# Kernel tuning notes

Hardware: AMD Instinct MI355X
Metric: run time of the kernel (lower is better)

## Reference

```python
import jax, jax.numpy as jnp
import numpy as np
import math

EMBED = 1024
HEADS = 16
HEAD_DIM = 64
HIDDEN = 4 * EMBED
EPS = 1e-5


def setup_inputs() -> dict:
    key = jax.random.key(0)
    ks = jax.random.split(key, 12)
    B, T, C = 2, 2048, EMBED
    s = 0.02
    return {
        "x": jax.random.normal(ks[0], (B, T, C), jnp.float32),
        "ln1_g": jnp.ones((C,), jnp.float32),
        "ln1_b": jnp.zeros((C,), jnp.float32),
        "qkv_w": jax.random.normal(ks[1], (C, 3 * C), jnp.float32) * s,
        "qkv_b": jnp.zeros((3 * C,), jnp.float32),
        "out_w": jax.random.normal(ks[2], (C, C), jnp.float32) * s,
        "out_b": jnp.zeros((C,), jnp.float32),
        "ln2_g": jnp.ones((C,), jnp.float32),
        "ln2_b": jnp.zeros((C,), jnp.float32),
        "fc1_w": jax.random.normal(ks[3], (C, HIDDEN), jnp.float32) * s,
        "fc1_b": jnp.zeros((HIDDEN,), jnp.float32),
        "fc2_w": jax.random.normal(ks[4], (HIDDEN, C), jnp.float32) * s,
        "fc2_b": jnp.zeros((C,), jnp.float32),
    }


def _layernorm(x, g, b):
    mu = jnp.mean(x, axis=-1, keepdims=True)
    var = jnp.var(x, axis=-1, keepdims=True)
    return (x - mu) * jax.lax.rsqrt(var + EPS) * g + b


def _attention(x, qkv_w, qkv_b, out_w, out_b):
    B, T, C = x.shape
    qkv = x @ qkv_w + qkv_b  # [B,T,3C]
    q, k, v = jnp.split(qkv, 3, axis=-1)
    # [B,H,T,hd]
    def heads(t):
        return t.reshape(B, T, HEADS, HEAD_DIM).transpose(0, 2, 1, 3)
    q, k, v = heads(q), heads(k), heads(v)
    scale = 1.0 / math.sqrt(HEAD_DIM)
    attn = jnp.einsum('bhqd,bhkd->bhqk', q, k) * scale
    causal = jnp.triu(jnp.ones((T, T), bool), k=1)
    attn = jnp.where(causal, -jnp.inf, attn)
    attn = jax.nn.softmax(attn, axis=-1)
    out = jnp.einsum('bhqk,bhkd->bhqd', attn, v)
    out = out.transpose(0, 2, 1, 3).reshape(B, T, C)
    return out @ out_w + out_b


def reference(x, ln1_g, ln1_b, qkv_w, qkv_b, out_w, out_b, ln2_g, ln2_b, fc1_w, fc1_b, fc2_w, fc2_b):
    x = x + _attention(_layernorm(x, ln1_g, ln1_b), qkv_w, qkv_b, out_w, out_b)
    h = _layernorm(x, ln2_g, ln2_b)
    h = jax.nn.gelu(h @ fc1_w + fc1_b, approximate=False) @ fc2_w + fc2_b
    return x + h
```

## Files before the change

kernel.cpp:

```cpp
#include <hip/hip_runtime.h>
#include <hip/hip_bf16.h>
#include <math.h>

typedef float f32x4 __attribute__((ext_vector_type(4)));
typedef __bf16 bf16x8 __attribute__((ext_vector_type(8)));
typedef __hip_bfloat16 bf16;

constexpr int T_SEQ = 2048;
constexpr int C_EMB = 1024;
constexpr int N_HEAD = 16;
constexpr int D_HEAD = 64;
constexpr int BATCH = 2;
constexpr int M_ROWS = BATCH * T_SEQ;
constexpr int HIDDEN_DIM = 4096;

static __device__ __forceinline__ f32x4 zero4() {
  f32x4 z; z[0] = 0.f; z[1] = 0.f; z[2] = 0.f; z[3] = 0.f; return z;
}

static __device__ __forceinline__ void gl_lds16(const bf16* g, bf16* l) {
  __builtin_amdgcn_global_load_lds(
      (const __attribute__((address_space(1))) unsigned int*)g,
      (__attribute__((address_space(3))) unsigned int*)l, 16, 0, 0);
}

#define BAR() asm volatile("s_barrier" ::: "memory")

__global__ __launch_bounds__(256) void ln_kernel(const float* __restrict__ x,
                                                 const float* __restrict__ gamma,
                                                 const float* __restrict__ beta,
                                                 bf16* __restrict__ out) {
  int row = blockIdx.x;
  const float* xr = x + (size_t)row * C_EMB;
  int t = threadIdx.x;
  float4 v = *(const float4*)&xr[t * 4];
  float s = v.x + v.y + v.z + v.w;
  float ss = v.x * v.x + v.y * v.y + v.z * v.z + v.w * v.w;
#pragma unroll
  for (int off = 32; off > 0; off >>= 1) {
    s += __shfl_down(s, off, 64);
    ss += __shfl_down(ss, off, 64);
  }
  __shared__ float sbuf[8];
  int w = t >> 6;
  if ((t & 63) == 0) { sbuf[w] = s; sbuf[4 + w] = ss; }
  __syncthreads();
  s = sbuf[0] + sbuf[1] + sbuf[2] + sbuf[3];
  ss = sbuf[4] + sbuf[5] + sbuf[6] + sbuf[7];
  float mu = s * (1.0f / C_EMB);
  float var = ss * (1.0f / C_EMB) - mu * mu;
  float rstd = rsqrtf(var + 1e-5f);
  float4 g4 = *(const float4*)&gamma[t * 4];
  float4 b4 = *(const float4*)&beta[t * 4];
  bf16* orow = out + (size_t)row * C_EMB + t * 4;
  orow[0] = __float2bfloat16((v.x - mu) * rstd * g4.x + b4.x);
  orow[1] = __float2bfloat16((v.y - mu) * rstd * g4.y + b4.y);
  orow[2] = __float2bfloat16((v.z - mu) * rstd * g4.z + b4.z);
  orow[3] = __float2bfloat16((v.w - mu) * rstd * g4.w + b4.w);
}

__global__ __launch_bounds__(256) void cast_transpose_all(
    const float* __restrict__ qkv_w, bf16* __restrict__ Wqkv,
    const float* __restrict__ out_w, bf16* __restrict__ Wout,
    const float* __restrict__ fc1_w, bf16* __restrict__ W1,
    const float* __restrict__ fc2_w, bf16* __restrict__ W2) {
  int id = blockIdx.x;
  const float* src; bf16* dst; int K, N, tt;
  if (id < 3072)      { src = qkv_w; dst = Wqkv; K = 1024; N = 3072; tt = id; }
  else if (id < 4096) { src = out_w; dst = Wout; K = 1024; N = 1024; tt = id - 3072; }
  else if (id < 8192) { src = fc1_w; dst = W1;   K = 1024; N = 4096; tt = id - 4096; }
  else                { src = fc2_w; dst = W2;   K = 4096; N = 1024; tt = id - 8192; }
  int ntx = N >> 5;
  int n0 = (tt % ntx) * 32, k0 = (tt / ntx) * 32;
  __shared__ float tile[32][33];
  int tx = threadIdx.x & 31, ty = threadIdx.x >> 5;
#pragma unroll
  for (int i = 0; i < 4; ++i)
    tile[ty + 8 * i][tx] = src[(size_t)(k0 + ty + 8 * i) * N + n0 + tx];
  __syncthreads();
#pragma unroll
  for (int i = 0; i < 4; ++i)
    dst[(size_t)(n0 + ty + 8 * i) * K + k0 + tx] = __float2bfloat16(tile[tx][ty + 8 * i]);
}

__global__ __launch_bounds__(256) void transpose_v(const bf16* __restrict__ V,
                                                   bf16* __restrict__ Vt) {
  int tt = blockIdx.x, bh = blockIdx.y;
  __shared__ bf16 tile[64][72];
  const bf16* src = V + ((size_t)bh * T_SEQ + tt * 64) * 64;
  int t = threadIdx.x;
  for (int idx = t; idx < 512; idx += 256) {
    int r = idx >> 3, c = (idx & 7) * 8;
    *(int4*)&tile[r][c] = *(const int4*)&src[r * 64 + c];
  }
  __syncthreads();
  bf16* dst = Vt + ((size_t)bh * 64) * T_SEQ + tt * 64;
  for (int idx = t; idx < 512; idx += 256) {
    int d = idx >> 3, c = (idx & 7) * 8;
    union { bf16 h[8]; int4 v; } u;
#pragma unroll
    for (int j = 0; j < 8; ++j) u.h[j] = tile[c + j][d];
    *(int4*)&dst[(size_t)d * T_SEQ + c] = u.v;
  }
}

template <int EPI>
__global__ __launch_bounds__(512) void gemm8p(
    const bf16* __restrict__ A, const bf16* __restrict__ Bt,
    const float* __restrict__ bias, int M, int N, int K,
    bf16* __restrict__ out_b16,
    bf16* __restrict__ q_out, bf16* __restrict__ k_out, bf16* __restrict__ v_out) {
  constexpr int NFR = 4;
  __shared__ bf16 Asl[2][2][128 * 64];
  __shared__ bf16 Bsl[2][2][128 * 64];

  int gx = gridDim.x, nwg = gx * gridDim.y;
  int flat = blockIdx.y * gx + blockIdx.x;
  int swz = (flat & 7) * (nwg >> 3) + (flat >> 3);
  int bx = swz % gx, by = swz / gx;

  int m0 = by * 256, n0 = bx * 256;
  int t = threadIdx.x;
  int wv = t >> 6, lane = t & 63, g = lane >> 4, r16 = lane & 15;
  int wm = wv >> 2, wn = wv & 3;

  f32x4 acc[8][NFR];
#pragma unroll
  for (int i = 0; i < 8; ++i)
#pragma unroll
    for (int j = 0; j < NFR; ++j) acc[i][j] = zero4();

  int lrow8 = lane >> 3;
  int srcg = (lane & 7) ^ lrow8;
  int NT = K / 64;

  auto stageA = [&](int tile, int h) {
    int par = tile & 1;
    const bf16* base = A + (size_t)(m0 + h * 128) * K + tile * 64;
#pragma unroll
    for (int j = 0; j < 2; ++j) {
      const bf16* src = base + (size_t)((wv * 2 + j) * 8 + lrow8) * K + srcg * 8;
      gl_lds16(src, &Asl[par][h][((wv * 2 + j) * 8) * 64]);
    }
  };
  auto stageB = [&](int tile, int h) {
    int par = tile & 1;
    const bf16* base = Bt + (size_t)(n0 + h * 128) * K + tile * 64;
#pragma unroll
    for (int j = 0; j < 2; ++j) {
      const bf16* src = base + (size_t)((wv * 2 + j) * 8 + lrow8) * K + srcg * 8;
      gl_lds16(src, &Bsl[par][h][((wv * 2 + j) * 8) * 64]);
    }
  };

  int xk[2];
#pragma unroll
  for (int kk = 0; kk < 2; ++kk) xk[kk] = (((kk * 4 + g) ^ (r16 & 7)) << 3);
  int bhalf = wn >> 1;
  int blrow0 = (wn & 1) * 64;

  stageA(0, 0); stageA(0, 1); stageB(0, 0); stageB(0, 1);
  if (NT > 1) {
    stageB(1, 0); stageB(1, 1);
    asm volatile("s_waitcnt vmcnt(4)" ::: "memory");
  } else {
    asm volatile("s_waitcnt vmcnt(0)" ::: "memory");
  }
  BAR();

  bf16x8 bfr[NFR][2];

  for (int u = 0; u < NT; ++u) {
    int par = u & 1;
    const bf16* Ab = &Asl[par][wm][0];
    const bf16* Bb = &Bsl[par][bhalf][0];
#pragma unroll
    for (int q = 0; q < 4; ++q) {
      if (q == 0) {
#pragma unroll
        for (int ni = 0; ni < NFR; ++ni)
#pragma unroll
          for (int kk = 0; kk < 2; ++kk)
            bfr[ni][kk] = *(const bf16x8*)&Bb[(blrow0 + ni * 16 + r16) * 64 + xk[kk]];
      }
      bf16x8 af[2][2];
#pragma unroll
      for (int d = 0; d < 2; ++d)
#pragma unroll
        for (int kk = 0; kk < 2; ++kk)
          af[d][kk] = *(const bf16x8*)&Ab[((2 * q + d) * 16 + r16) * 64 + xk[kk]];
      if (q == 0) { if (u + 1 < NT) stageA(u + 1, 0); }
      else if (q == 1) { if (u + 1 < NT) stageA(u + 1, 1); }
      else if (q == 2) { if (u + 2 < NT) stageB(u + 2, 0); }
      else { if (u + 2 < NT) stageB(u + 2, 1); }
      BAR();
      asm volatile("s_waitcnt lgkmcnt(0)" ::: "memory");
      __builtin_amdgcn_sched_barrier(0);
      __builtin_amdgcn_s_setprio(1);
#pragma unroll
      for (int d = 0; d < 2; ++d)
#pragma unroll
        for (int ni = 0; ni < NFR; ++ni) {
          acc[2 * q + d][ni] = __builtin_amdgcn_mfma_f32_16x16x32_bf16(af[d][0], bfr[ni][0], acc[2 * q + d][ni], 0, 0, 0);
          acc[2 * q + d][ni] = __builtin_amdgcn_mfma_f32_16x16x32_bf16(af[d][1], bfr[ni][1], acc[2 * q + d][ni], 0, 0, 0);
        }
      __builtin_amdgcn_s_setprio(0);
      if (q == 3) {
        if (u + 2 < NT)
          asm volatile("s_waitcnt vmcnt(4)" ::: "memory");
        else
          asm volatile("s_waitcnt vmcnt(0)" ::: "memory");
      }
      BAR();
    }
  }

#pragma unroll
  for (int mi = 0; mi < 8; ++mi) {
#pragma unroll
    for (int ni = 0; ni < NFR; ++ni) {
      int col = n0 + wn * 64 + ni * 16 + r16;
      float bv = bias[col];
#pragma unroll
      for (int reg = 0; reg < 4; ++reg) {
        int row = m0 + wm * 128 + mi * 16 + g * 4 + reg;
        float v = acc[mi][ni][reg] + bv;
        if constexpr (EPI == 0) {
          int part = col >> 10, cc = col & 1023;
          int hh = cc >> 6, dd = cc & 63;
          int bb = row >> 11, tt2 = row & 2047;
          size_t idx = (((size_t)bb * N_HEAD + hh) * T_SEQ + tt2) * D_HEAD + dd;
          if (part == 0) q_out[idx] = __float2bfloat16(v * 0.125f);
          else if (part == 1) k_out[idx] = __float2bfloat16(v);
          else v_out[idx] = __float2bfloat16(v);
        } else {
          float ge = 0.5f * v * (1.0f + erff(v * 0.70710678118f));
          out_b16[(size_t)row * N + col] = __float2bfloat16(ge);
        }
      }
    }
  }
}

__global__ __launch_bounds__(256) void gemmW(
    const bf16* __restrict__ A, const bf16* __restrict__ Bt,
    const float* __restrict__ bias, int M, int N, int K,
    const float* __restrict__ res, float* __restrict__ out_f32) {
  __shared__ bf16 Abuf[2][128 * 64];
  __shared__ bf16 Bbuf[2][64 * 64];

  int gx = gridDim.x, nwg = gx * gridDim.y;
  int flat = blockIdx.y * gx + blockIdx.x;
  int swz = (flat & 7) * (nwg >> 3) + (flat >> 3);
  int bx = swz % gx, by = swz / gx;

  int m0 = by * 128, n0 = bx * 64;
  int t = threadIdx.x;
  int wv = t >> 6, lane = t & 63, g = lane >> 4, r16 = lane & 15;
  int wm = wv >> 1, wn = wv & 1;

  f32x4 acc[4][2];
#pragma unroll
  for (int i = 0; i < 4; ++i)
#pragma unroll
    for (int j = 0; j < 2; ++j) acc[i][j] = zero4();

  int lrow8 = lane >> 3;
  int srcg = (lane & 7) ^ lrow8;
  int NT = K / 64;

  const bf16* gAp[4];
  const bf16* gBp[2];
#pragma unroll
  for (int i = 0; i < 4; ++i)
    gAp[i] = A + (size_t)(m0 + (wv * 4 + i) * 8 + lrow8) * K + srcg * 8;
#pragma unroll
  for (int i = 0; i < 2; ++i)
    gBp[i] = Bt + (size_t)(n0 + (wv * 2 + i) * 8 + lrow8) * K + srcg * 8;

  int aoff[4], boff[2], xk[2];
#pragma unroll
  for (int mi = 0; mi < 4; ++mi) aoff[mi] = (wm * 64 + mi * 16 + r16) * 64;
#pragma unroll
  for (int ni = 0; ni < 2; ++ni) boff[ni] = (wn * 32 + ni * 16 + r16) * 64;
#pragma unroll
  for (int kk = 0; kk < 2; ++kk) xk[kk] = (((kk * 4 + g) ^ (r16 & 7)) << 3);

  auto stage = [&](int buf) {
#pragma unroll
    for (int i = 0; i < 4; ++i) {
      gl_lds16(gAp[i], &Abuf[buf][((wv * 4 + i) * 8) * 64]);
      gAp[i] += 64;
    }
#pragma unroll
    for (int i = 0; i < 2; ++i) {
      gl_lds16(gBp[i], &Bbuf[buf][((wv * 2 + i) * 8) * 64]);
      gBp[i] += 64;
    }
  };

  auto compute = [&](int buf) {
    const bf16* Ab = &Abuf[buf][0];
    const bf16* Bb = &Bbuf[buf][0];
    bf16x8 bfr[2][2];
#pragma unroll
    for (int ni = 0; ni < 2; ++ni)
#pragma unroll
      for (int kk = 0; kk < 2; ++kk)
        bfr[ni][kk] = *(const bf16x8*)&Bb[boff[ni] + xk[kk]];
#pragma unroll
    for (int mi = 0; mi < 4; ++mi) {
      bf16x8 a0 = *(const bf16x8*)&Ab[aoff[mi] + xk[0]];
      bf16x8 a1 = *(const bf16x8*)&Ab[aoff[mi] + xk[1]];
#pragma unroll
      for (int ni = 0; ni < 2; ++ni) {
        acc[mi][ni] = __builtin_amdgcn_mfma_f32_16x16x32_bf16(a0, bfr[ni][0], acc[mi][ni], 0, 0, 0);
        acc[mi][ni] = __builtin_amdgcn_mfma_f32_16x16x32_bf16(a1, bfr[ni][1], acc[mi][ni], 0, 0, 0);
      }
    }
  };

  stage(0);
  __syncthreads();
  for (int tt2 = 0; tt2 < NT; ++tt2) {
    int cur = tt2 & 1;
    if (tt2 + 1 < NT) stage(cur ^ 1);
    compute(cur);
    __syncthreads();
  }

#pragma unroll
  for (int mi = 0; mi < 4; ++mi) {
#pragma unroll
    for (int ni = 0; ni < 2; ++ni) {
      int col = n0 + wn * 32 + ni * 16 + r16;
      float bv = bias[col];
#pragma unroll
      for (int reg = 0; reg < 4; ++reg) {
        int row = m0 + wm * 64 + mi * 16 + g * 4 + reg;
        size_t idx = (size_t)row * N + col;
        out_f32[idx] = acc[mi][ni][reg] + bv + res[idx];
      }
    }
  }
}

__global__ __launch_bounds__(256) void attn_kernel(const bf16* __restrict__ Q,
                                                   const bf16* __restrict__ Kg,
                                                   const bf16* __restrict__ Vt,
                                                   bf16* __restrict__ O) {
  constexpr int NQ = T_SEQ / 64;
  int p = blockIdx.x, bh = blockIdx.y;
  int qtA = p, qtB = NQ - 1 - p;
  int b = bh >> 4, h = bh & 15;
  __shared__ bf16 Ks[2][64 * 64];
  __shared__ bf16 Vs[2][64 * 64];
  __shared__ bf16 Ps[4][16 * 64];
  int t = threadIdx.x, w = t >> 6, lane = t & 63, g = lane >> 4, r16 = lane & 15;

  const bf16* QpA = Q + ((size_t)bh * T_SEQ + qtA * 64) * 64;
  const bf16* QpB = Q + ((size_t)bh * T_SEQ + qtB * 64) * 64;
  bf16x8 qfA[2], qfB[2];
#pragma unroll
  for (int kk = 0; kk < 2; ++kk) {
    qfA[kk] = *(const bf16x8*)&QpA[(w * 16 + r16) * 64 + kk * 32 + g * 8];
    qfB[kk] = *(const bf16x8*)&QpB[(w * 16 + r16) * 64 + kk * 32 + g * 8];
  }

  float lsA[4] = {0.f, 0.f, 0.f, 0.f}, lsB[4] = {0.f, 0.f, 0.f, 0.f};
  f32x4 oA[4], oB[4];
#pragma unroll
  for (int i = 0; i < 4; ++i) { oA[i] = zero4(); oB[i] = zero4(); }

  bf16* Psw = Ps[w];

  int sg0 = w * 128 + lane, sg1 = w * 128 + 64 + lane;
  int sr0 = sg0 >> 3, sc0 = (sg0 & 7) ^ (sr0 & 7);
  int sr1 = sg1 >> 3, sc1 = (sg1 & 7) ^ (sr1 & 7);

  auto stage = [&](int kt, int buf) {
    const bf16* Kp = Kg + ((size_t)bh * T_SEQ + kt * 64) * 64;
    const bf16* Vp = Vt + (size_t)bh * 64 * T_SEQ + kt * 64;
    gl_lds16(Kp + sr0 * 64 + sc0 * 8, &Ks[buf][(w * 128) * 8]);
    gl_lds16(Vp + (size_t)sr0 * T_SEQ + sc0 * 8, &Vs[buf][(w * 128) * 8]);
    gl_lds16(Kp + sr1 * 64 + sc1 * 8, &Ks[buf][(w * 128 + 64) * 8]);
    gl_lds16(Vp + (size_t)sr1 * T_SEQ + sc1 * 8, &Vs[buf][(w * 128 + 64) * 8]);
  };

  auto process = [&](const bf16x8* qf, float* ls, f32x4* o_acc, bool diag,
                     const bf16* Ksb, const bf16* Vsb) {
    f32x4 s[4];
#pragma unroll
    for (int ni = 0; ni < 4; ++ni) {
      s[ni] = zero4();
#pragma unroll
      for (int kk = 0; kk < 2; ++kk) {
        bf16x8 kf = *(const bf16x8*)&Ksb[(ni * 16 + r16) * 64 + (((kk * 4 + g) ^ (r16 & 7)) << 3)];
        s[ni] = __builtin_amdgcn_mfma_f32_16x16x32_bf16(qf[kk], kf, s[ni], 0, 0, 0);
      }
    }
    if (diag) {
#pragma unroll
      for (int ni = 0; ni < 4; ++ni) {
        int kl = ni * 16 + r16;
#pragma unroll
        for (int reg = 0; reg < 4; ++reg) {
          int ql = w * 16 + g * 4 + reg;
          if (kl > ql) s[ni][reg] = -1e30f;
        }
      }
    }
#pragma unroll
    for (int ni = 0; ni < 4; ++ni) {
#pragma unroll
      for (int reg = 0; reg < 4; ++reg) {
        float pv = __expf(s[ni][reg]);
        s[ni][reg] = pv;
        ls[reg] += pv;
        int rr = g * 4 + reg;
        Psw[rr * 64 + (((ni * 2 + (r16 >> 3)) ^ (rr & 7)) << 3) + (r16 & 7)] =
            __float2bfloat16(pv);
      }
    }
    bf16x8 pf[2];
#pragma unroll
    for (int kk = 0; kk < 2; ++kk)
      pf[kk] = *(const bf16x8*)&Psw[r16 * 64 + (((kk * 4 + g) ^ (r16 & 7)) << 3)];
#pragma unroll
    for (int nd = 0; nd < 4; ++nd)
#pragma unroll
      for (int kk = 0; kk < 2; ++kk) {
        bf16x8 vf = *(const bf16x8*)&Vsb[(nd * 16 + r16) * 64 + (((kk * 4 + g) ^ (r16 & 7)) << 3)];
        o_acc[nd] = __builtin_amdgcn_mfma_f32_16x16x32_bf16(pf[kk], vf, o_acc[nd], 0, 0, 0);
      }
  };

  stage(0, 0);
  __syncthreads();
  for (int kt = 0; kt <= qtB; ++kt) {
    int cur = kt & 1;
    if (kt + 1 <= qtB) stage(kt + 1, cur ^ 1);
    process(qfB, lsB, oB, kt == qtB, &Ks[cur][0], &Vs[cur][0]);
    if (kt <= qtA) process(qfA, lsA, oA, kt == qtA, &Ks[cur][0], &Vs[cur][0]);
    __syncthreads();
  }

#pragma unroll
  for (int reg = 0; reg < 4; ++reg) {
#pragma unroll
    for (int off = 1; off < 16; off <<= 1) {
      lsA[reg] += __shfl_xor(lsA[reg], off, 64);
      lsB[reg] += __shfl_xor(lsB[reg], off, 64);
    }
  }
#pragma unroll
  for (int reg = 0; reg < 4; ++reg) {
    float invA = 1.0f / lsA[reg];
    float invB = 1.0f / lsB[reg];
    int rowA = b * T_SEQ + qtA * 64 + w * 16 + g * 4 + reg;
    int rowB = b * T_SEQ + qtB * 64 + w * 16 + g * 4 + reg;
#pragma unroll
    for (int nd = 0; nd < 4; ++nd) {
      int col = h * 64 + nd * 16 + r16;
      O[(size_t)rowA * C_EMB + col] = __float2bfloat16(oA[nd][reg] * invA);
      O[(size_t)rowB * C_EMB + col] = __float2bfloat16(oB[nd][reg] * invB);
    }
  }
}

extern "C" void kernel_launch(void* const* d_in, const int* in_sizes, int n_in,
                              void* d_out, int out_size, void* d_ws, size_t ws_size,
                              hipStream_t stream) {
  (void)in_sizes; (void)n_in; (void)out_size; (void)ws_size;
  const float* x     = (const float*)d_in[0];
  const float* ln1_g = (const float*)d_in[1];
  const float* ln1_b = (const float*)d_in[2];
  const float* qkv_w = (const float*)d_in[3];
  const float* qkv_b = (const float*)d_in[4];
  const float* out_w = (const float*)d_in[5];
  const float* out_b = (const float*)d_in[6];
  const float* ln2_g = (const float*)d_in[7];
  const float* ln2_b = (const float*)d_in[8];
  const float* fc1_w = (const float*)d_in[9];
  const float* fc1_b = (const float*)d_in[10];
  const float* fc2_w = (const float*)d_in[11];
  const float* fc2_b = (const float*)d_in[12];
  float* out = (float*)d_out;

  char* ws = (char*)d_ws;
  size_t off = 0;
  auto alloc = [&](size_t bytes) {
    void* p = ws + off;
    off += (bytes + 255) & ~(size_t)255;
    return p;
  };
  bf16* Wqkv = (bf16*)alloc((size_t)3 * C_EMB * C_EMB * 2);
  bf16* Wout = (bf16*)alloc((size_t)C_EMB * C_EMB * 2);
  bf16* W1   = (bf16*)alloc((size_t)HIDDEN_DIM * C_EMB * 2);
  bf16* W2   = (bf16*)alloc((size_t)C_EMB * HIDDEN_DIM * 2);
  float* x2  = (float*)alloc((size_t)M_ROWS * C_EMB * 4);
  bf16* Xb   = (bf16*)alloc((size_t)M_ROWS * C_EMB * 2);
  bf16* Qb   = (bf16*)alloc((size_t)M_ROWS * C_EMB * 2 * 4);
  bf16* Kb   = Qb + (size_t)M_ROWS * C_EMB;
  bf16* Vb   = Kb + (size_t)M_ROWS * C_EMB;
  bf16* Vtb  = Vb + (size_t)M_ROWS * C_EMB;
  bf16* H1   = Qb;

  cast_transpose_all<<<12288, 256, 0, stream>>>(qkv_w, Wqkv, out_w, Wout,
                                                fc1_w, W1, fc2_w, W2);

  ln_kernel<<<M_ROWS, 256, 0, stream>>>(x, ln1_g, ln1_b, Xb);

  gemm8p<0><<<dim3(3 * C_EMB / 256, M_ROWS / 256), 512, 0, stream>>>(
      Xb, Wqkv, qkv_b, M_ROWS, 3 * C_EMB, C_EMB,
      nullptr, Qb, Kb, Vb);

  transpose_v<<<dim3(T_SEQ / 64, BATCH * N_HEAD), 256, 0, stream>>>(Vb, Vtb);

  attn_kernel<<<dim3(T_SEQ / 128, BATCH * N_HEAD), 256, 0, stream>>>(Qb, Kb, Vtb, Xb);

  gemmW<<<dim3(C_EMB / 64, M_ROWS / 128), 256, 0, stream>>>(
      Xb, Wout, out_b, M_ROWS, C_EMB, C_EMB, x, x2);

  ln_kernel<<<M_ROWS, 256, 0, stream>>>(x2, ln2_g, ln2_b, Xb);

  gemm8p<2><<<dim3(HIDDEN_DIM / 256, M_ROWS / 256), 512, 0, stream>>>(
      Xb, W1, fc1_b, M_ROWS, HIDDEN_DIM, C_EMB,
      H1, nullptr, nullptr, nullptr);

  gemmW<<<dim3(C_EMB / 64, M_ROWS / 128), 256, 0, stream>>>(
      H1, W2, fc2_b, M_ROWS, C_EMB, HIDDEN_DIM, x2, out);
}
```

Baseline: 233.8 us.

## Fuse weight cast with LN1, write V transposed from QKV GEMM, retile FC1

Merges the weight cast-transpose kernel and the first layernorm into one launch. The QKV GEMM epilogue now writes V directly in transposed layout, which removes the separate transpose_v kernel and its extra pass over V. FC1 moves from the 256x256 8-wave GEMM to a new 128x128 4-wave GEMM with a larger grid, and H1 gets its own buffer. The transposed V stores are strided in T, so that epilogue's writes are poorly coalesced, and the smaller FC1 tile reuses operands less.

```diff
diff --git a/kernel.cpp b/kernel.cpp
--- a/kernel.cpp
+++ b/kernel.cpp
@@ -25,6 +25,62 @@
 }
 
 #define BAR() asm volatile("s_barrier" ::: "memory")
+
+__global__ __launch_bounds__(256) void preproc(
+    const float* __restrict__ qkv_w, bf16* __restrict__ Wqkv,
+    const float* __restrict__ out_w, bf16* __restrict__ Wout,
+    const float* __restrict__ fc1_w, bf16* __restrict__ W1,
+    const float* __restrict__ fc2_w, bf16* __restrict__ W2,
+    const float* __restrict__ x, const float* __restrict__ gamma,
+    const float* __restrict__ beta, bf16* __restrict__ xb) {
+  __shared__ float smem[32 * 33];
+  int id = blockIdx.x;
+  int t = threadIdx.x;
+  if (id >= 12288) {
+    int row = id - 12288;
+    const float* xr = x + (size_t)row * C_EMB;
+    float4 v = *(const float4*)&xr[t * 4];
+    float s = v.x + v.y + v.z + v.w;
+    float ss = v.x * v.x + v.y * v.y + v.z * v.z + v.w * v.w;
+#pragma unroll
+    for (int off = 32; off > 0; off >>= 1) {
+      s += __shfl_down(s, off, 64);
+      ss += __shfl_down(ss, off, 64);
+    }
+    int w = t >> 6;
+    if ((t & 63) == 0) { smem[w] = s; smem[4 + w] = ss; }
+    __syncthreads();
+    s = smem[0] + smem[1] + smem[2] + smem[3];
+    ss = smem[4] + smem[5] + smem[6] + smem[7];
+    float mu = s * (1.0f / C_EMB);
+    float var = ss * (1.0f / C_EMB) - mu * mu;
+    float rstd = rsqrtf(var + 1e-5f);
+    float4 g4 = *(const float4*)&gamma[t * 4];
+    float4 b4 = *(const float4*)&beta[t * 4];
+    bf16* orow = xb + (size_t)row * C_EMB + t * 4;
+    orow[0] = __float2bfloat16((v.x - mu) * rstd * g4.x + b4.x);
+    orow[1] = __float2bfloat16((v.y - mu) * rstd * g4.y + b4.y);
+    orow[2] = __float2bfloat16((v.z - mu) * rstd * g4.z + b4.z);
+    orow[3] = __float2bfloat16((v.w - mu) * rstd * g4.w + b4.w);
+    return;
+  }
+  const float* src; bf16* dst; int K, N, tt;
+  if (id < 3072)      { src = qkv_w; dst = Wqkv; K = 1024; N = 3072; tt = id; }
+  else if (id < 4096) { src = out_w; dst = Wout; K = 1024; N = 1024; tt = id - 3072; }
+  else if (id < 8192) { src = fc1_w; dst = W1;   K = 1024; N = 4096; tt = id - 4096; }
+  else                { src = fc2_w; dst = W2;   K = 4096; N = 1024; tt = id - 8192; }
+  int ntx = N >> 5;
+  int n0 = (tt % ntx) * 32, k0 = (tt / ntx) * 32;
+  float (*tile)[33] = (float(*)[33])smem;
+  int tx = t & 31, ty = t >> 5;
+#pragma unroll
+  for (int i = 0; i < 4; ++i)
+    tile[ty + 8 * i][tx] = src[(size_t)(k0 + ty + 8 * i) * N + n0 + tx];
+  __syncthreads();
+#pragma unroll
+  for (int i = 0; i < 4; ++i)
+    dst[(size_t)(n0 + ty + 8 * i) * K + k0 + tx] = __float2bfloat16(tile[tx][ty + 8 * i]);
+}
 
 __global__ __launch_bounds__(256) void ln_kernel(const float* __restrict__ x,
                                                  const float* __restrict__ gamma,
@@ -59,57 +115,12 @@
   orow[3] = __float2bfloat16((v.w - mu) * rstd * g4.w + b4.w);
 }
 
-__global__ __launch_bounds__(256) void cast_transpose_all(
-    const float* __restrict__ qkv_w, bf16* __restrict__ Wqkv,
-    const float* __restrict__ out_w, bf16* __restrict__ Wout,
-    const float* __restrict__ fc1_w, bf16* __restrict__ W1,
-    const float* __restrict__ fc2_w, bf16* __restrict__ W2) {
-  int id = blockIdx.x;
-  const float* src; bf16* dst; int K, N, tt;
-  if (id < 3072)      { src = qkv_w; dst = Wqkv; K = 1024; N = 3072; tt = id; }
-  else if (id < 4096) { src = out_w; dst = Wout; K = 1024; N = 1024; tt = id - 3072; }
-  else if (id < 8192) { src = fc1_w; dst = W1;   K = 1024; N = 4096; tt = id - 4096; }
-  else                { src = fc2_w; dst = W2;   K = 4096; N = 1024; tt = id - 8192; }
-  int ntx = N >> 5;
-  int n0 = (tt % ntx) * 32, k0 = (tt / ntx) * 32;
-  __shared__ float tile[32][33];
-  int tx = threadIdx.x & 31, ty = threadIdx.x >> 5;
-#pragma unroll
-  for (int i = 0; i < 4; ++i)
-    tile[ty + 8 * i][tx] = src[(size_t)(k0 + ty + 8 * i) * N + n0 + tx];
-  __syncthreads();
-#pragma unroll
-  for (int i = 0; i < 4; ++i)
-    dst[(size_t)(n0 + ty + 8 * i) * K + k0 + tx] = __float2bfloat16(tile[tx][ty + 8 * i]);
-}
-
-__global__ __launch_bounds__(256) void transpose_v(const bf16* __restrict__ V,
-                                                   bf16* __restrict__ Vt) {
-  int tt = blockIdx.x, bh = blockIdx.y;
-  __shared__ bf16 tile[64][72];
-  const bf16* src = V + ((size_t)bh * T_SEQ + tt * 64) * 64;
-  int t = threadIdx.x;
-  for (int idx = t; idx < 512; idx += 256) {
-    int r = idx >> 3, c = (idx & 7) * 8;
-    *(int4*)&tile[r][c] = *(const int4*)&src[r * 64 + c];
-  }
-  __syncthreads();
-  bf16* dst = Vt + ((size_t)bh * 64) * T_SEQ + tt * 64;
-  for (int idx = t; idx < 512; idx += 256) {
-    int d = idx >> 3, c = (idx & 7) * 8;
-    union { bf16 h[8]; int4 v; } u;
-#pragma unroll
-    for (int j = 0; j < 8; ++j) u.h[j] = tile[c + j][d];
-    *(int4*)&dst[(size_t)d * T_SEQ + c] = u.v;
-  }
-}
-
 template <int EPI>
 __global__ __launch_bounds__(512) void gemm8p(
     const bf16* __restrict__ A, const bf16* __restrict__ Bt,
     const float* __restrict__ bias, int M, int N, int K,
     bf16* __restrict__ out_b16,
-    bf16* __restrict__ q_out, bf16* __restrict__ k_out, bf16* __restrict__ v_out) {
+    bf16* __restrict__ q_out, bf16* __restrict__ k_out, bf16* __restrict__ vt_out) {
   constexpr int NFR = 4;
   __shared__ bf16 Asl[2][2][128 * 64];
   __shared__ bf16 Bsl[2][2][128 * 64];
@@ -229,10 +240,123 @@
           int part = col >> 10, cc = col & 1023;
           int hh = cc >> 6, dd = cc & 63;
           int bb = row >> 11, tt2 = row & 2047;
-          size_t idx = (((size_t)bb * N_HEAD + hh) * T_SEQ + tt2) * D_HEAD + dd;
-          if (part == 0) q_out[idx] = __float2bfloat16(v * 0.125f);
-          else if (part == 1) k_out[idx] = __float2bfloat16(v);
-          else v_out[idx] = __float2bfloat16(v);
+          if (part == 0) {
+            size_t idx = (((size_t)bb * N_HEAD + hh) * T_SEQ + tt2) * D_HEAD + dd;
+            q_out[idx] = __float2bfloat16(v * 0.125f);
+          } else if (part == 1) {
+            size_t idx = (((size_t)bb * N_HEAD + hh) * T_SEQ + tt2) * D_HEAD + dd;
+            k_out[idx] = __float2bfloat16(v);
+          } else {
+            size_t idx = (((size_t)bb * N_HEAD + hh) * D_HEAD + dd) * T_SEQ + tt2;
+            vt_out[idx] = __float2bfloat16(v);
+          }
+        } else {
+          float ge = 0.5f * v * (1.0f + erff(v * 0.70710678118f));
+          out_b16[(size_t)row * N + col] = __float2bfloat16(ge);
+        }
+      }
+    }
+  }
+}
+
+template <int EPI>
+__global__ __launch_bounds__(256) void gemmW128(
+    const bf16* __restrict__ A, const bf16* __restrict__ Bt,
+    const float* __restrict__ bias, int M, int N, int K,
+    const float* __restrict__ res, float* __restrict__ out_f32,
+    bf16* __restrict__ out_b16) {
+  __shared__ bf16 Abuf[2][128 * 64];
+  __shared__ bf16 Bbuf[2][128 * 64];
+
+  int gx = gridDim.x, nwg = gx * gridDim.y;
+  int flat = blockIdx.y * gx + blockIdx.x;
+  int swz = (flat & 7) * (nwg >> 3) + (flat >> 3);
+  int bx = swz % gx, by = swz / gx;
+
+  int m0 = by * 128, n0 = bx * 128;
+  int t = threadIdx.x;
+  int wv = t >> 6, lane = t & 63, g = lane >> 4, r16 = lane & 15;
+  int wm = wv >> 1, wn = wv & 1;
+
+  f32x4 acc[4][4];
+#pragma unroll
+  for (int i = 0; i < 4; ++i)
+#pragma unroll
+    for (int j = 0; j < 4; ++j) acc[i][j] = zero4();
+
+  int lrow8 = lane >> 3;
+  int srcg = (lane & 7) ^ lrow8;
+  int NT = K / 64;
+
+  const bf16* gAp[4];
+  const bf16* gBp[4];
+#pragma unroll
+  for (int i = 0; i < 4; ++i) {
+    gAp[i] = A + (size_t)(m0 + (wv * 4 + i) * 8 + lrow8) * K + srcg * 8;
+    gBp[i] = Bt + (size_t)(n0 + (wv * 4 + i) * 8 + lrow8) * K + srcg * 8;
+  }
+
+  int aoff[4], boff[4], xk[2];
+#pragma unroll
+  for (int mi = 0; mi < 4; ++mi) aoff[mi] = (wm * 64 + mi * 16 + r16) * 64;
+#pragma unroll
+  for (int ni = 0; ni < 4; ++ni) boff[ni] = (wn * 64 + ni * 16 + r16) * 64;
+#pragma unroll
+  for (int kk = 0; kk < 2; ++kk) xk[kk] = (((kk * 4 + g) ^ (r16 & 7)) << 3);
+
+  auto stage = [&](int buf) {
+#pragma unroll
+    for (int i = 0; i < 4; ++i) {
+      gl_lds16(gAp[i], &Abuf[buf][((wv * 4 + i) * 8) * 64]);
+      gAp[i] += 64;
+      gl_lds16(gBp[i], &Bbuf[buf][((wv * 4 + i) * 8) * 64]);
+      gBp[i] += 64;
+    }
+  };
+
+  auto compute = [&](int buf) {
+    const bf16* Ab = &Abuf[buf][0];
+    const bf16* Bb = &Bbuf[buf][0];
+    bf16x8 bfr[4][2];
+#pragma unroll
+    for (int ni = 0; ni < 4; ++ni)
+#pragma unroll
+      for (int kk = 0; kk < 2; ++kk)
+        bfr[ni][kk] = *(const bf16x8*)&Bb[boff[ni] + xk[kk]];
+#pragma unroll
+    for (int mi = 0; mi < 4; ++mi) {
+      bf16x8 a0 = *(const bf16x8*)&Ab[aoff[mi] + xk[0]];
+      bf16x8 a1 = *(const bf16x8*)&Ab[aoff[mi] + xk[1]];
+#pragma unroll
+      for (int ni = 0; ni < 4; ++ni) {
+        acc[mi][ni] = __builtin_amdgcn_mfma_f32_16x16x32_bf16(a0, bfr[ni][0], acc[mi][ni], 0, 0, 0);
+        acc[mi][ni] = __builtin_amdgcn_mfma_f32_16x16x32_bf16(a1, bfr[ni][1], acc[mi][ni], 0, 0, 0);
+      }
+    }
+  };
+
+  stage(0);
+  __syncthreads();
+  for (int tt2 = 0; tt2 < NT; ++tt2) {
+    int cur = tt2 & 1;
+    if (tt2 + 1 < NT) stage(cur ^ 1);
+    compute(cur);
+    __syncthreads();
+  }
+
+#pragma unroll
+  for (int mi = 0; mi < 4; ++mi) {
+#pragma unroll
+    for (int ni = 0; ni < 4; ++ni) {
+      int col = n0 + wn * 64 + ni * 16 + r16;
+      float bv = bias[col];
+#pragma unroll
+      for (int reg = 0; reg < 4; ++reg) {
+        int row = m0 + wm * 64 + mi * 16 + g * 4 + reg;
+        float v = acc[mi][ni][reg] + bv;
+        if constexpr (EPI == 1) {
+          size_t idx = (size_t)row * N + col;
+          out_f32[idx] = v + res[idx];
         } else {
           float ge = 0.5f * v * (1.0f + erff(v * 0.70710678118f));
           out_b16[(size_t)row * N + col] = __float2bfloat16(ge);
@@ -500,22 +624,17 @@
   bf16* W2   = (bf16*)alloc((size_t)C_EMB * HIDDEN_DIM * 2);
   float* x2  = (float*)alloc((size_t)M_ROWS * C_EMB * 4);
   bf16* Xb   = (bf16*)alloc((size_t)M_ROWS * C_EMB * 2);
-  bf16* Qb   = (bf16*)alloc((size_t)M_ROWS * C_EMB * 2 * 4);
+  bf16* Qb   = (bf16*)alloc((size_t)M_ROWS * C_EMB * 2 * 3);
   bf16* Kb   = Qb + (size_t)M_ROWS * C_EMB;
-  bf16* Vb   = Kb + (size_t)M_ROWS * C_EMB;
-  bf16* Vtb  = Vb + (size_t)M_ROWS * C_EMB;
-  bf16* H1   = Qb;
-
-  cast_transpose_all<<<12288, 256, 0, stream>>>(qkv_w, Wqkv, out_w, Wout,
-                                                fc1_w, W1, fc2_w, W2);
-
-  ln_kernel<<<M_ROWS, 256, 0, stream>>>(x, ln1_g, ln1_b, Xb);
+  bf16* Vtb  = Kb + (size_t)M_ROWS * C_EMB;
+  bf16* H1   = (bf16*)alloc((size_t)M_ROWS * HIDDEN_DIM * 2);
+
+  preproc<<<16384, 256, 0, stream>>>(qkv_w, Wqkv, out_w, Wout, fc1_w, W1, fc2_w, W2,
+                                     x, ln1_g, ln1_b, Xb);
 
   gemm8p<0><<<dim3(3 * C_EMB / 256, M_ROWS / 256), 512, 0, stream>>>(
       Xb, Wqkv, qkv_b, M_ROWS, 3 * C_EMB, C_EMB,
-      nullptr, Qb, Kb, Vb);
-
-  transpose_v<<<dim3(T_SEQ / 64, BATCH * N_HEAD), 256, 0, stream>>>(Vb, Vtb);
+      nullptr, Qb, Kb, Vtb);
 
   attn_kernel<<<dim3(T_SEQ / 128, BATCH * N_HEAD), 256, 0, stream>>>(Qb, Kb, Vtb, Xb);
 
@@ -524,9 +643,9 @@
 
   ln_kernel<<<M_ROWS, 256, 0, stream>>>(x2, ln2_g, ln2_b, Xb);
 
-  gemm8p<2><<<dim3(HIDDEN_DIM / 256, M_ROWS / 256), 512, 0, stream>>>(
+  gemmW128<2><<<dim3(HIDDEN_DIM / 128, M_ROWS / 128), 256, 0, stream>>>(
       Xb, W1, fc1_b, M_ROWS, HIDDEN_DIM, C_EMB,
-      H1, nullptr, nullptr, nullptr);
+      nullptr, nullptr, H1);
 
   gemmW<<<dim3(C_EMB / 64, M_ROWS / 128), 256, 0, stream>>>(
       H1, W2, fc2_b, M_ROWS, C_EMB, HIDDEN_DIM, x2, out);
```

After: 256.4 us. +9.6%, slower.
